# Optimization experiments

Measured on AMD Instinct MI355X. Metric: run time of the kernel, lower is better.

The kernel has to match this reference:

```python
import jax, jax.numpy as jnp
import numpy as np
import math

H = 8  # num_heads
SCALE = 1.0 / math.sqrt(512.0)  # original divides by sqrt(dim_V), not sqrt(head_dim)


def setup_inputs() -> dict:
    key = jax.random.key(0)
    ks = jax.random.split(key, 16)
    B, N, D = 32, 512, 512
    s = 1.0 / math.sqrt(D)
    return {
        "Q": jax.random.normal(ks[0], (B, N, D), jnp.float32),
        "K": jax.random.normal(ks[1], (B, N, D), jnp.float32),
        "Wq": jax.random.normal(ks[2], (D, D), jnp.float32) * s,
        "bq": jnp.zeros((D,), jnp.float32),
        "Wk": jax.random.normal(ks[3], (D, D), jnp.float32) * s,
        "bk": jnp.zeros((D,), jnp.float32),
        "Wv": jax.random.normal(ks[4], (D, D), jnp.float32) * s,
        "bv": jnp.zeros((D,), jnp.float32),
        "Wo": jax.random.normal(ks[5], (D, D), jnp.float32) * s,
        "bo": jnp.zeros((D,), jnp.float32),
        "W1": jax.random.normal(ks[6], (D, D), jnp.float32) * s,
        "b1": jnp.zeros((D,), jnp.float32),
        "W2": jax.random.normal(ks[7], (D, D), jnp.float32) * s,
        "b2": jnp.zeros((D,), jnp.float32),
    }


def reference(Q, K, Wq, bq, Wk, bk, Wv, bv, Wo, bo, W1, b1, W2, b2):
    B, Nq, D = Q.shape
    dh = D // H
    # projections (torch Linear: x @ W.T + b)
    q = (Q @ Wq.T + bq).reshape(B, Nq, H, dh)
    k = (K @ Wk.T + bk).reshape(B, K.shape[1], H, dh)
    v = (K @ Wv.T + bv).reshape(B, K.shape[1], H, dh)
    # scores: [B, H, Nq, Nk], scaled by 1/sqrt(dim_V)
    scores = jnp.einsum("bqhd,bkhd->bhqk", q, k) * SCALE
    # NOTE: original softmax is over dim=1 of [H*B, Nq, Nk] == the QUERY axis
    A = jax.nn.softmax(scores, axis=2)
    attn = jnp.einsum("bhqk,bkhd->bqhd", A, v).reshape(B, Nq, D)
    out = Q + (attn @ Wo.T + bo)  # dropout p=0.0
    ffn = jax.nn.relu(out @ W1.T + b1) @ W2.T + b2
    return out + ffn
```

## Files before the change

kernel.cpp:

```cpp
#include <hip/hip_runtime.h>
#include <stdint.h>

#define SCALE_ 0.044194173824159216f
#define QSC_ (0.044194173824159216f * 1.4426950408889634f)

typedef __attribute__((ext_vector_type(8))) short bf16x8;
typedef __attribute__((ext_vector_type(4))) float f32x4;
typedef __attribute__((ext_vector_type(16))) float f32x16;
typedef __attribute__((ext_vector_type(2))) unsigned int uint2v;

__device__ __forceinline__ ushort f2b(float f) {
  union { float f; uint32_t u; } v; v.f = f;
  return (ushort)((v.u + 0x7fffu + ((v.u >> 16) & 1u)) >> 16);
}
__device__ __forceinline__ uint32_t cvtpk(float lo, float hi) {
  uint32_t r; asm("v_cvt_pk_bf16_f32 %0, %1, %2" : "=v"(r) : "v"(lo), "v"(hi)); return r;
}
__device__ __forceinline__ float ex2(float x) {
  float r; asm("v_exp_f32 %0, %1" : "=v"(r) : "v"(x)); return r;
}
__device__ __forceinline__ void gld16(void* lds, const void* g) {
  __builtin_amdgcn_global_load_lds(
      (const __attribute__((address_space(1))) uint32_t*)g,
      (__attribute__((address_space(3))) uint32_t*)lds, 16, 0, 0);
}

__global__ __launch_bounds__(256)
void k_cvtw(const float* __restrict__ w0, const float* __restrict__ w1,
            const float* __restrict__ w2, const float* __restrict__ w3,
            const float* __restrict__ w4, const float* __restrict__ w5,
            ushort* __restrict__ Wb)
{
  const int NW = 262144;
  int i = (blockIdx.x * 256 + threadIdx.x) * 4;
  int seg = i >> 18;
  int off = i & (NW - 1);
  const float* src;
  switch (seg) { case 0: src = w0; break; case 1: src = w1; break; case 2: src = w2; break;
                 case 3: src = w3; break; case 4: src = w4; break; default: src = w5; }
  float4 v = *(const float4*)(src + off);
  ushort4 o = make_ushort4(f2b(v.x), f2b(v.y), f2b(v.z), f2b(v.w));
  *(ushort4*)(Wb + (size_t)seg * NW + off) = o;
}

template<int EPI>
__device__ __forceinline__ void gemm_body(const ushort* __restrict__ A, const ushort* __restrict__ Bw,
                                          const float* __restrict__ bias, const float* __restrict__ extra,
                                          float* __restrict__ outf, ushort* __restrict__ outb,
                                          char* lds, int m0, int n0)
{
  const int t = threadIdx.x;
  const int w = t >> 6, lane = t & 63;
  const int wm = w >> 1, wn = w & 1;
  const int rA = lane & 15, g = lane >> 4;

  const ushort* srcA[4]; int ldsA[4];
#pragma unroll
  for (int j = 0; j < 4; j++) {
    int L = (t + j*512) * 16;
    int U = L ^ (((L >> 7) & 7) << 4);
    srcA[j] = A + (size_t)(m0 + (U >> 7))*512 + ((U & 127) >> 1);
    ldsA[j] = L;
  }
  const ushort* srcB[2]; int ldsB[2];
#pragma unroll
  for (int j = 0; j < 2; j++) {
    int L = (t + j*512) * 16;
    int U = L ^ (((L >> 7) & 7) << 4);
    srcB[j] = Bw + (size_t)(n0 + (U >> 7))*512 + ((U & 127) >> 1);
    ldsB[j] = 32768 + L;
  }

#define STAGE_T(ti) do { char* bb_ = lds + ((ti) % 3) * 49152; \
    _Pragma("unroll") \
    for (int j = 0; j < 4; j++) gld16(bb_ + ldsA[j], srcA[j] + (ti)*64); \
    _Pragma("unroll") \
    for (int j = 0; j < 2; j++) gld16(bb_ + ldsB[j], srcB[j] + (ti)*64); } while (0)

  STAGE_T(0); STAGE_T(1);

  f32x4 acc[4][4] = {};
  for (int i = 0; i < 8; i++) {
    if (i < 7) asm volatile("s_waitcnt vmcnt(6)" ::: "memory");
    else       asm volatile("s_waitcnt vmcnt(0)" ::: "memory");
    __builtin_amdgcn_s_barrier();
    __builtin_amdgcn_sched_barrier(0);
    const char* bufc = lds + (i % 3) * 49152;

    bf16x8 afA[4], bfA[4], afB[4], bfB[4];
#pragma unroll
    for (int m = 0; m < 4; m++) {
      int row = wm*64 + m*16 + rA;
      afA[m] = *(const bf16x8*)(bufc + ((row*128 + g*16) ^ ((row & 7) << 4)));
      afB[m] = *(const bf16x8*)(bufc + ((row*128 + 64 + g*16) ^ ((row & 7) << 4)));
    }
#pragma unroll
    for (int n = 0; n < 4; n++) {
      int row = wn*64 + n*16 + rA;
      bfA[n] = *(const bf16x8*)(bufc + 32768 + ((row*128 + g*16) ^ ((row & 7) << 4)));
      bfB[n] = *(const bf16x8*)(bufc + 32768 + ((row*128 + 64 + g*16) ^ ((row & 7) << 4)));
    }
    if (i < 6) STAGE_T(i + 2);
    __builtin_amdgcn_sched_barrier(0);
    __builtin_amdgcn_s_setprio(1);
#pragma unroll
    for (int m = 0; m < 4; m++)
#pragma unroll
      for (int n = 0; n < 4; n++)
        acc[m][n] = __builtin_amdgcn_mfma_f32_16x16x32_bf16(afA[m], bfA[n], acc[m][n], 0, 0, 0);
#pragma unroll
    for (int m = 0; m < 4; m++)
#pragma unroll
      for (int n = 0; n < 4; n++)
        acc[m][n] = __builtin_amdgcn_mfma_f32_16x16x32_bf16(afB[m], bfB[n], acc[m][n], 0, 0, 0);
    __builtin_amdgcn_s_setprio(0);
  }
#undef STAGE_T

#pragma unroll
  for (int m = 0; m < 4; m++)
#pragma unroll
    for (int n = 0; n < 4; n++) {
      int col = n0 + wn*64 + n*16 + rA;
      float bb = bias[col];
#pragma unroll
      for (int r = 0; r < 4; r++) {
        int row = m0 + wm*64 + m*16 + g*4 + r;
        size_t idx = (size_t)row*512 + col;
        float v = acc[m][n][r] + bb;
        if (EPI == 1)      { float o = extra[idx] + v; outf[idx] = o; outb[idx] = f2b(o); }
        else if (EPI == 2) outb[idx] = f2b(v > 0.f ? v : 0.f);
        else               outf[idx] += v;
      }
    }
}

template<int EPI>
__global__ __launch_bounds__(512, 2)
void k_gemm(const ushort* __restrict__ A, const ushort* __restrict__ Bw,
            const float* __restrict__ bias, const float* __restrict__ extra,
            float* __restrict__ outf, ushort* __restrict__ outb)
{
  __shared__ __align__(16) char lds[3*49152];
  gemm_body<EPI>(A, Bw, bias, extra, outf, outb, lds, blockIdx.x*256, blockIdx.y*128);
}

template<int DUAL>
__device__ __forceinline__ void proj_body(const float* __restrict__ A32, const ushort* __restrict__ B0w,
                                          const ushort* __restrict__ B1w,
                                          const float* __restrict__ bias0, const float* __restrict__ bias1,
                                          ushort* __restrict__ out0, ushort* __restrict__ vpT,
                                          char* lds, int m0, int n0, float os)
{
  const int t = threadIdx.x;
  const int w = t >> 6, lane = t & 63;
  const int wm = w >> 1, wn = w & 1;
  const int rA = lane & 15, g = lane >> 4;
  const int BUF = DUAL ? 49152 : 40960;
  const int L = DUAL ? 6 : 5;

  const float* srcA[4]; int ldsA[4];
#pragma unroll
  for (int j = 0; j < 4; j++) {
    int Lb = (t + j*512) * 16;
    int U = Lb ^ (((Lb >> 7) & 7) << 4);
    srcA[j] = A32 + (size_t)(m0 + (U >> 7))*512 + ((U & 127) >> 2);
    ldsA[j] = Lb;
  }
  const ushort* srcB0; const ushort* srcB1; int ldsB;
  {
    int Lb = t * 16;
    int U = Lb ^ (((Lb >> 6) & 3) << 4);
    int row = U >> 6, col = (U & 63) >> 1;
    srcB0 = B0w + (size_t)(n0 + row)*512 + col;
    srcB1 = DUAL ? (B1w + (size_t)(n0 + row)*512 + col) : srcB0;
    ldsB = 32768 + Lb;
  }

#define PSTAGE(ti) do { char* bb_ = lds + ((ti) % 3) * BUF; \
    _Pragma("unroll") \
    for (int j = 0; j < 4; j++) gld16(bb_ + ldsA[j], srcA[j] + (ti)*32); \
    gld16(bb_ + ldsB, srcB0 + (ti)*32); \
    if (DUAL) gld16(bb_ + 8192 + ldsB, srcB1 + (ti)*32); } while (0)

  PSTAGE(0); PSTAGE(1);

  f32x4 acc0[4][4] = {};
  f32x4 acc1[4][4] = {};
  for (int i = 0; i < 16; i++) {
    if (i < 15) { if (DUAL) asm volatile("s_waitcnt vmcnt(6)" ::: "memory");
                  else      asm volatile("s_waitcnt vmcnt(5)" ::: "memory"); }
    else          asm volatile("s_waitcnt vmcnt(0)" ::: "memory");
    __builtin_amdgcn_s_barrier();
    __builtin_amdgcn_sched_barrier(0);
    const char* bufc = lds + (i % 3) * BUF;

    bf16x8 af[4];
#pragma unroll
    for (int m = 0; m < 4; m++) {
      int row = wm*64 + m*16 + rA;
      int o0 = (row*128 + g*32) ^ ((row & 7) << 4);
      f32x4 lo = *(const f32x4*)(bufc + o0);
      f32x4 hi = *(const f32x4*)(bufc + (o0 ^ 16));
      union { uint32_t u[4]; bf16x8 v; } af_;
      af_.u[0] = cvtpk(lo[0], lo[1]); af_.u[1] = cvtpk(lo[2], lo[3]);
      af_.u[2] = cvtpk(hi[0], hi[1]); af_.u[3] = cvtpk(hi[2], hi[3]);
      af[m] = af_.v;
    }
    bf16x8 bf0[4];
#pragma unroll
    for (int n = 0; n < 4; n++) {
      int row = wn*64 + n*16 + rA;
      bf0[n] = *(const bf16x8*)(bufc + 32768 + ((row*64 + g*16) ^ ((row & 3) << 4)));
    }
    if (i < 14) PSTAGE(i + 2);
    __builtin_amdgcn_sched_barrier(0);
    __builtin_amdgcn_s_setprio(1);
#pragma unroll
    for (int m = 0; m < 4; m++)
#pragma unroll
      for (int n = 0; n < 4; n++)
        acc0[m][n] = __builtin_amdgcn_mfma_f32_16x16x32_bf16(af[m], bf0[n], acc0[m][n], 0, 0, 0);
    __builtin_amdgcn_s_setprio(0);
    if (DUAL) {
      bf16x8 bf1[4];
#pragma unroll
      for (int n = 0; n < 4; n++) {
        int row = wn*64 + n*16 + rA;
        bf1[n] = *(const bf16x8*)(bufc + 40960 + ((row*64 + g*16) ^ ((row & 3) << 4)));
      }
      __builtin_amdgcn_s_setprio(1);
#pragma unroll
      for (int m = 0; m < 4; m++)
#pragma unroll
        for (int n = 0; n < 4; n++)
          acc1[m][n] = __builtin_amdgcn_mfma_f32_16x16x32_bf16(af[m], bf1[n], acc1[m][n], 0, 0, 0);
      __builtin_amdgcn_s_setprio(0);
    }
  }
#undef PSTAGE

#pragma unroll
  for (int m = 0; m < 4; m++)
#pragma unroll
    for (int n = 0; n < 4; n++) {
      int col = n0 + wn*64 + n*16 + rA;
      {
        float bb = bias0[col];
#pragma unroll
        for (int r = 0; r < 4; r++) {
          int row = m0 + wm*64 + m*16 + g*4 + r;
          out0[(size_t)row*512 + col] = f2b((acc0[m][n][r] + bb) * os);
        }
      }
      if (DUAL) {
        float bb = bias1[col];
        int b = m0 >> 9, k0 = m0 & 511;
        int hh = col >> 6, dl = col & 63;
        int kg = k0 + wm*64 + m*16 + g*4;
        float v0 = acc1[m][n][0] + bb, v1 = acc1[m][n][1] + bb;
        float v2 = acc1[m][n][2] + bb, v3 = acc1[m][n][3] + bb;
        uint2 pk;
        pk.x = (uint32_t)f2b(v0) | ((uint32_t)f2b(v1) << 16);
        pk.y = (uint32_t)f2b(v2) | ((uint32_t)f2b(v3) << 16);
        *(uint2*)(vpT + ((size_t)((b*8 + hh)*64 + dl)*512 + kg)) = pk;
      }
    }
}

__global__ __launch_bounds__(512, 1)
void k_projq(const float* __restrict__ Qf, const ushort* __restrict__ Wb,
             const float* __restrict__ bq, ushort* __restrict__ qp)
{
  __shared__ __align__(16) char lds[3*40960];
  proj_body<0>(Qf, Wb, nullptr, bq, nullptr, qp, nullptr,
               lds, blockIdx.x*256, blockIdx.y*128, QSC_);
}

__global__ __launch_bounds__(512, 1)
void k_projkv(const float* __restrict__ Kf, const ushort* __restrict__ Wb,
              const float* __restrict__ bk, const float* __restrict__ bvv,
              ushort* __restrict__ kp, ushort* __restrict__ vpT)
{
  __shared__ __align__(16) char lds[3*49152];
  proj_body<1>(Kf, Wb + (size_t)262144, Wb + 2*(size_t)262144, bk, bvv, kp, vpT,
               lds, blockIdx.x*256, blockIdx.y*128, 1.0f);
}

__global__ __launch_bounds__(512, 2)
void k_att2(const ushort* __restrict__ qp, const ushort* __restrict__ kp,
            const ushort* __restrict__ vpT, float* __restrict__ zinv,
            ushort* __restrict__ attn)
{
  __shared__ __align__(16) char kt[65536];
  __shared__ __align__(16) char vt[65536];
  __shared__ __align__(16) char qpr[32768];
  int bh = blockIdx.x;
  int b = bh >> 3, h = bh & 7;
  int t = threadIdx.x, w = t >> 6, lane = t & 63;
  int rA = lane & 15, g = lane >> 4;
  const ushort* kbase = kp + (size_t)(b*512)*512 + h*64;
  const ushort* qbase = qp + (size_t)(b*512)*512 + h*64;
  const ushort* vbase = vpT + (size_t)bh*64*512;

#pragma unroll
  for (int i = 0; i < 8; i++) {
    int c = i*512 + t; int row = c >> 3, sl = c & 7;
    gld16(kt + c*16, kbase + (size_t)row*512 + ((sl ^ (row & 7))*8));
  }
#define STAGE_Q(buf, qb) do { \
    _Pragma("unroll") \
    for (int i = 0; i < 2; i++) { \
      int c = i*512 + t; int row = c >> 3, sl = c & 7; \
      gld16(qpr + (buf)*16384 + c*16, \
            qbase + (size_t)((qb)*128 + row)*512 + ((sl ^ (row & 7))*8)); } } while (0)
  STAGE_Q(0, 0);
  STAGE_Q(1, 1);
#pragma unroll
  for (int i = 0; i < 8; i++) {
    int c = i*512 + t; int d = c >> 6, sl = c & 63;
    gld16(vt + c*16, vbase + (size_t)d*512 + ((sl ^ (d & 7))*8));
  }

  asm volatile("s_waitcnt vmcnt(10)" ::: "memory");
  __builtin_amdgcn_s_barrier();
  __builtin_amdgcn_sched_barrier(0);
  bf16x8 kf[4][2];
#pragma unroll
  for (int n = 0; n < 4; n++)
#pragma unroll
    for (int ks = 0; ks < 2; ks++) {
      int k = w*64 + n*16 + rA;
      kf[n][ks] = *(const bf16x8*)(kt + k*128 + (((ks*4 + g) ^ (k & 7))*16));
    }
  float Zacc[4] = {0.f, 0.f, 0.f, 0.f};
  for (int qb = 0; qb < 4; qb++) {
    if (qb == 1)      { asm volatile("s_waitcnt vmcnt(10)" ::: "memory"); }
    else if (qb == 2) { asm volatile("s_waitcnt vmcnt(2)" ::: "memory"); }
    else if (qb == 3) { asm volatile("s_waitcnt vmcnt(0)" ::: "memory"); }
    if (qb) { __builtin_amdgcn_s_barrier(); __builtin_amdgcn_sched_barrier(0); }
    const char* qtb = qpr + (qb & 1)*16384;
    f32x4 acc[8][4] = {};
#pragma unroll
    for (int ks = 0; ks < 2; ks++) {
      bf16x8 af[8];
#pragma unroll
      for (int m = 0; m < 8; m++) {
        int q = m*16 + rA;
        af[m] = *(const bf16x8*)(qtb + q*128 + (((ks*4 + g) ^ (q & 7))*16));
      }
      __builtin_amdgcn_s_setprio(1);
#pragma unroll
      for (int m = 0; m < 8; m++)
#pragma unroll
        for (int n = 0; n < 4; n++)
          acc[m][n] = __builtin_amdgcn_mfma_f32_16x16x32_bf16(af[m], kf[n][ks], acc[m][n], 0, 0, 0);
      __builtin_amdgcn_s_setprio(0);
    }
    if (qb < 3) __builtin_amdgcn_s_barrier();
    if (qb < 2) STAGE_Q(qb & 1, qb + 2);
#pragma unroll
    for (int m = 0; m < 8; m++)
#pragma unroll
      for (int n = 0; n < 4; n++) {
        float s = 0.f;
#pragma unroll
        for (int r = 0; r < 4; r++) s += ex2(acc[m][n][r]);
        Zacc[n] += s;
      }
  }
#undef STAGE_Q
#pragma unroll
  for (int n = 0; n < 4; n++) {
    float v = Zacc[n];
    v += __shfl_xor(v, 16);
    v += __shfl_xor(v, 32);
    if (lane < 16) ((float*)qpr)[w*64 + n*16 + lane] = 1.0f / v;
  }
  __syncthreads();

  const int l31 = lane & 31, hi5 = lane >> 5;
  bf16x8 qf2[2][4];
#pragma unroll
  for (int qb = 0; qb < 2; qb++)
#pragma unroll
    for (int ksd = 0; ksd < 4; ksd++)
      qf2[qb][ksd] = *(const bf16x8*)(qbase + (size_t)(w*64 + qb*32 + l31)*512 + ksd*16 + hi5*8);
  const float* zl = (const float*)qpr;
  f32x16 oacc[2][2] = {};
  for (int kc = 0; kc < 16; kc++) {
    bf16x8 kf2[4];
#pragma unroll
    for (int ksd = 0; ksd < 4; ksd++) {
      int k = kc*32 + l31;
      kf2[ksd] = *(const bf16x8*)(kt + k*128 + (((ksd*2 + hi5) ^ (k & 7))*16));
    }
    bf16x8 vf2[2][2];
#pragma unroll
    for (int db = 0; db < 2; db++)
#pragma unroll
      for (int ks = 0; ks < 2; ks++) {
        int d = db*32 + l31;
        vf2[db][ks] = *(const bf16x8*)(vt + d*1024 + (((kc*4 + ks*2 + hi5) ^ (d & 7))*16));
      }
    f32x4 zv[4];
#pragma unroll
    for (int j = 0; j < 4; j++)
      zv[j] = *(const f32x4*)(zl + kc*32 + j*8 + hi5*4);
#pragma unroll
    for (int qb = 0; qb < 2; qb++) {
      f32x16 s = {};
      __builtin_amdgcn_s_setprio(1);
#pragma unroll
      for (int ksd = 0; ksd < 4; ksd++)
        s = __builtin_amdgcn_mfma_f32_32x32x16_bf16(kf2[ksd], qf2[qb][ksd], s, 0, 0, 0);
      __builtin_amdgcn_s_setprio(0);
      float e[16];
#pragma unroll
      for (int r = 0; r < 16; r++) e[r] = ex2(s[r]) * zv[r >> 2][r & 3];
      uint32_t x0 = cvtpk(e[0], e[1]),   y0 = cvtpk(e[4], e[5]);
      uint32_t x1 = cvtpk(e[2], e[3]),   y1 = cvtpk(e[6], e[7]);
      uint32_t x2 = cvtpk(e[8], e[9]),   y2 = cvtpk(e[12], e[13]);
      uint32_t x3 = cvtpk(e[10], e[11]), y3 = cvtpk(e[14], e[15]);
      uint2v r0 = __builtin_amdgcn_permlane32_swap(x0, y0, false, false);
      uint2v r1 = __builtin_amdgcn_permlane32_swap(x1, y1, false, false);
      uint2v r2 = __builtin_amdgcn_permlane32_swap(x2, y2, false, false);
      uint2v r3 = __builtin_amdgcn_permlane32_swap(x3, y3, false, false);
      union { uint32_t u[4]; bf16x8 v; } p0, p1;
      p0.u[0] = r0[0]; p0.u[1] = r1[0]; p0.u[2] = r0[1]; p0.u[3] = r1[1];
      p1.u[0] = r2[0]; p1.u[1] = r3[0]; p1.u[2] = r2[1]; p1.u[3] = r3[1];
      __builtin_amdgcn_s_setprio(1);
#pragma unroll
      for (int db = 0; db < 2; db++) {
        oacc[qb][db] = __builtin_amdgcn_mfma_f32_32x32x16_bf16(p0.v, vf2[db][0], oacc[qb][db], 0, 0, 0);
        oacc[qb][db] = __builtin_amdgcn_mfma_f32_32x32x16_bf16(p1.v, vf2[db][1], oacc[qb][db], 0, 0, 0);
      }
      __builtin_amdgcn_s_setprio(0);
    }
  }
#pragma unroll
  for (int qb = 0; qb < 2; qb++)
#pragma unroll
    for (int db = 0; db < 2; db++)
#pragma unroll
      for (int r = 0; r < 16; r++) {
        int q = w*64 + qb*32 + (r & 3) + 8*(r >> 2) + 4*hi5;
        int d = db*32 + l31;
        attn[(size_t)(b*512 + q)*512 + h*64 + d] = f2b(oacc[qb][db][r]);
      }
}

extern "C" void kernel_launch(void* const* d_in, const int* in_sizes, int n_in,
                              void* d_out, int out_size, void* d_ws, size_t ws_size,
                              hipStream_t stream) {
  const float* Q  = (const float*)d_in[0];
  const float* K  = (const float*)d_in[1];
  const float* Wq = (const float*)d_in[2];
  const float* bq = (const float*)d_in[3];
  const float* Wk = (const float*)d_in[4];
  const float* bk = (const float*)d_in[5];
  const float* Wv = (const float*)d_in[6];
  const float* bv = (const float*)d_in[7];
  const float* Wo = (const float*)d_in[8];
  const float* bo = (const float*)d_in[9];
  const float* W1 = (const float*)d_in[10];
  const float* b1 = (const float*)d_in[11];
  const float* W2 = (const float*)d_in[12];
  const float* b2 = (const float*)d_in[13];
  float* out = (float*)d_out;

  const size_t SZ = (size_t)16384 * 512;
  ushort* attn = (ushort*)d_ws;
  ushort* outb = attn + SZ;
  ushort* qp   = outb + SZ;
  ushort* kp   = qp + SZ;
  ushort* vpT  = kp + SZ;
  ushort* Wb   = vpT + SZ;
  float*  zinv = (float*)(Wb + 6 * (size_t)262144);
  ushort* h1   = vpT;

  k_cvtw<<<dim3(1536), dim3(256), 0, stream>>>(Wq, Wk, Wv, Wo, W1, W2, Wb);
  k_projq<<<dim3(64, 4), dim3(512), 0, stream>>>(Q, Wb, bq, qp);
  k_projkv<<<dim3(64, 4), dim3(512), 0, stream>>>(K, Wb, bk, bv, kp, vpT);
  k_att2<<<dim3(256), dim3(512), 0, stream>>>(qp, kp, vpT, zinv, attn);
  k_gemm<1><<<dim3(64, 4), dim3(512), 0, stream>>>(attn, Wb + 3*(size_t)262144, bo, Q, out, outb);
  k_gemm<2><<<dim3(64, 4), dim3(512), 0, stream>>>(outb, Wb + 4*(size_t)262144, b1, nullptr, nullptr, h1);
  k_gemm<3><<<dim3(64, 4), dim3(512), 0, stream>>>(h1, Wb + 5*(size_t)262144, b2, nullptr, out, nullptr);
}
```

Measured before the change: 141.7 us.

## Merge Q/KV projection launches, read Q/V from global in attention, retune B swizzle

Fuses the Q and KV projection kernels into one launch with a z dimension, so both projections can run concurrently across the GPU. The attention kernel drops its LDS staging of Q and V. It now loads those fragments straight from global memory, with only K and the normalizer kept in LDS, which cuts shared memory use and may allow more resident blocks. The B-tile LDS swizzle in the projection is changed to use a different row bit pattern to reduce bank conflicts. The risk is that the global loads in the attention inner loops are uncoalesced and uncached, adding latency.

```diff
diff --git a/kernel.cpp b/kernel.cpp
--- a/kernel.cpp
+++ b/kernel.cpp
@@ -157,7 +157,6 @@
   const int wm = w >> 1, wn = w & 1;
   const int rA = lane & 15, g = lane >> 4;
   const int BUF = DUAL ? 49152 : 40960;
-  const int L = DUAL ? 6 : 5;
 
   const float* srcA[4]; int ldsA[4];
 #pragma unroll
@@ -170,7 +169,7 @@
   const ushort* srcB0; const ushort* srcB1; int ldsB;
   {
     int Lb = t * 16;
-    int U = Lb ^ (((Lb >> 6) & 3) << 4);
+    int U = Lb ^ (((Lb >> 7) & 3) << 4);
     int row = U >> 6, col = (U & 63) >> 1;
     srcB0 = B0w + (size_t)(n0 + row)*512 + col;
     srcB1 = DUAL ? (B1w + (size_t)(n0 + row)*512 + col) : srcB0;
@@ -211,7 +210,7 @@
 #pragma unroll
     for (int n = 0; n < 4; n++) {
       int row = wn*64 + n*16 + rA;
-      bf0[n] = *(const bf16x8*)(bufc + 32768 + ((row*64 + g*16) ^ ((row & 3) << 4)));
+      bf0[n] = *(const bf16x8*)(bufc + 32768 + ((row*64 + g*16) ^ (((row >> 1) & 3) << 4)));
     }
     if (i < 14) PSTAGE(i + 2);
     __builtin_amdgcn_sched_barrier(0);
@@ -227,7 +226,7 @@
 #pragma unroll
       for (int n = 0; n < 4; n++) {
         int row = wn*64 + n*16 + rA;
-        bf1[n] = *(const bf16x8*)(bufc + 40960 + ((row*64 + g*16) ^ ((row & 3) << 4)));
+        bf1[n] = *(const bf16x8*)(bufc + 40960 + ((row*64 + g*16) ^ (((row >> 1) & 3) << 4)));
       }
       __builtin_amdgcn_s_setprio(1);
 #pragma unroll
@@ -269,32 +268,28 @@
 }
 
 __global__ __launch_bounds__(512, 1)
-void k_projq(const float* __restrict__ Qf, const ushort* __restrict__ Wb,
-             const float* __restrict__ bq, ushort* __restrict__ qp)
-{
-  __shared__ __align__(16) char lds[3*40960];
-  proj_body<0>(Qf, Wb, nullptr, bq, nullptr, qp, nullptr,
-               lds, blockIdx.x*256, blockIdx.y*128, QSC_);
-}
-
-__global__ __launch_bounds__(512, 1)
-void k_projkv(const float* __restrict__ Kf, const ushort* __restrict__ Wb,
-              const float* __restrict__ bk, const float* __restrict__ bvv,
-              ushort* __restrict__ kp, ushort* __restrict__ vpT)
+void k_proj(const float* __restrict__ Qf, const float* __restrict__ Kf,
+            const ushort* __restrict__ Wb,
+            const float* __restrict__ bq, const float* __restrict__ bk,
+            const float* __restrict__ bvv,
+            ushort* __restrict__ qp, ushort* __restrict__ kp, ushort* __restrict__ vpT)
 {
   __shared__ __align__(16) char lds[3*49152];
-  proj_body<1>(Kf, Wb + (size_t)262144, Wb + 2*(size_t)262144, bk, bvv, kp, vpT,
-               lds, blockIdx.x*256, blockIdx.y*128, 1.0f);
+  if (blockIdx.z == 0) {
+    proj_body<0>(Qf, Wb, nullptr, bq, nullptr, qp, nullptr,
+                 lds, blockIdx.x*256, blockIdx.y*128, QSC_);
+  } else {
+    proj_body<1>(Kf, Wb + (size_t)262144, Wb + 2*(size_t)262144, bk, bvv, kp, vpT,
+                 lds, blockIdx.x*256, blockIdx.y*128, 1.0f);
+  }
 }
 
 __global__ __launch_bounds__(512, 2)
 void k_att2(const ushort* __restrict__ qp, const ushort* __restrict__ kp,
-            const ushort* __restrict__ vpT, float* __restrict__ zinv,
-            ushort* __restrict__ attn)
+            const ushort* __restrict__ vpT, ushort* __restrict__ attn)
 {
   __shared__ __align__(16) char kt[65536];
-  __shared__ __align__(16) char vt[65536];
-  __shared__ __align__(16) char qpr[32768];
+  __shared__ __align__(16) float zl[512];
   int bh = blockIdx.x;
   int b = bh >> 3, h = bh & 7;
   int t = threadIdx.x, w = t >> 6, lane = t & 63;
@@ -308,23 +303,10 @@
     int c = i*512 + t; int row = c >> 3, sl = c & 7;
     gld16(kt + c*16, kbase + (size_t)row*512 + ((sl ^ (row & 7))*8));
   }
-#define STAGE_Q(buf, qb) do { \
-    _Pragma("unroll") \
-    for (int i = 0; i < 2; i++) { \
-      int c = i*512 + t; int row = c >> 3, sl = c & 7; \
-      gld16(qpr + (buf)*16384 + c*16, \
-            qbase + (size_t)((qb)*128 + row)*512 + ((sl ^ (row & 7))*8)); } } while (0)
-  STAGE_Q(0, 0);
-  STAGE_Q(1, 1);
-#pragma unroll
-  for (int i = 0; i < 8; i++) {
-    int c = i*512 + t; int d = c >> 6, sl = c & 63;
-    gld16(vt + c*16, vbase + (size_t)d*512 + ((sl ^ (d & 7))*8));
-  }
-
-  asm volatile("s_waitcnt vmcnt(10)" ::: "memory");
+  asm volatile("s_waitcnt vmcnt(0)" ::: "memory");
   __builtin_amdgcn_s_barrier();
   __builtin_amdgcn_sched_barrier(0);
+
   bf16x8 kf[4][2];
 #pragma unroll
   for (int n = 0; n < 4; n++)
@@ -334,20 +316,16 @@
       kf[n][ks] = *(const bf16x8*)(kt + k*128 + (((ks*4 + g) ^ (k & 7))*16));
     }
   float Zacc[4] = {0.f, 0.f, 0.f, 0.f};
+#pragma unroll 1
   for (int qb = 0; qb < 4; qb++) {
-    if (qb == 1)      { asm volatile("s_waitcnt vmcnt(10)" ::: "memory"); }
-    else if (qb == 2) { asm volatile("s_waitcnt vmcnt(2)" ::: "memory"); }
-    else if (qb == 3) { asm volatile("s_waitcnt vmcnt(0)" ::: "memory"); }
-    if (qb) { __builtin_amdgcn_s_barrier(); __builtin_amdgcn_sched_barrier(0); }
-    const char* qtb = qpr + (qb & 1)*16384;
     f32x4 acc[8][4] = {};
 #pragma unroll
     for (int ks = 0; ks < 2; ks++) {
       bf16x8 af[8];
 #pragma unroll
       for (int m = 0; m < 8; m++) {
-        int q = m*16 + rA;
-        af[m] = *(const bf16x8*)(qtb + q*128 + (((ks*4 + g) ^ (q & 7))*16));
+        int q = qb*128 + m*16 + rA;
+        af[m] = *(const bf16x8*)(qbase + (size_t)q*512 + ks*32 + g*8);
       }
       __builtin_amdgcn_s_setprio(1);
 #pragma unroll
@@ -357,8 +335,6 @@
           acc[m][n] = __builtin_amdgcn_mfma_f32_16x16x32_bf16(af[m], kf[n][ks], acc[m][n], 0, 0, 0);
       __builtin_amdgcn_s_setprio(0);
     }
-    if (qb < 3) __builtin_amdgcn_s_barrier();
-    if (qb < 2) STAGE_Q(qb & 1, qb + 2);
 #pragma unroll
     for (int m = 0; m < 8; m++)
 #pragma unroll
@@ -369,13 +345,12 @@
         Zacc[n] += s;
       }
   }
-#undef STAGE_Q
 #pragma unroll
   for (int n = 0; n < 4; n++) {
     float v = Zacc[n];
     v += __shfl_xor(v, 16);
     v += __shfl_xor(v, 32);
-    if (lane < 16) ((float*)qpr)[w*64 + n*16 + lane] = 1.0f / v;
+    if (lane < 16) zl[w*64 + n*16 + lane] = 1.0f / v;
   }
   __syncthreads();
 
@@ -386,8 +361,8 @@
 #pragma unroll
     for (int ksd = 0; ksd < 4; ksd++)
       qf2[qb][ksd] = *(const bf16x8*)(qbase + (size_t)(w*64 + qb*32 + l31)*512 + ksd*16 + hi5*8);
-  const float* zl = (const float*)qpr;
   f32x16 oacc[2][2] = {};
+#pragma unroll 1
   for (int kc = 0; kc < 16; kc++) {
     bf16x8 kf2[4];
 #pragma unroll
@@ -401,12 +376,12 @@
 #pragma unroll
       for (int ks = 0; ks < 2; ks++) {
         int d = db*32 + l31;
-        vf2[db][ks] = *(const bf16x8*)(vt + d*1024 + (((kc*4 + ks*2 + hi5) ^ (d & 7))*16));
+        vf2[db][ks] = *(const bf16x8*)(vbase + (size_t)d*512 + kc*32 + ks*16 + hi5*8);
       }
     f32x4 zv[4];
 #pragma unroll
     for (int j = 0; j < 4; j++)
-      zv[j] = *(const f32x4*)(zl + kc*32 + j*8 + hi5*4);
+      zv[j] = *(const f32x4*)(&zl[kc*32 + j*8 + hi5*4]);
 #pragma unroll
     for (int qb = 0; qb < 2; qb++) {
       f32x16 s = {};
@@ -476,13 +451,11 @@
   ushort* kp   = qp + SZ;
   ushort* vpT  = kp + SZ;
   ushort* Wb   = vpT + SZ;
-  float*  zinv = (float*)(Wb + 6 * (size_t)262144);
   ushort* h1   = vpT;
 
   k_cvtw<<<dim3(1536), dim3(256), 0, stream>>>(Wq, Wk, Wv, Wo, W1, W2, Wb);
-  k_projq<<<dim3(64, 4), dim3(512), 0, stream>>>(Q, Wb, bq, qp);
-  k_projkv<<<dim3(64, 4), dim3(512), 0, stream>>>(K, Wb, bk, bv, kp, vpT);
-  k_att2<<<dim3(256), dim3(512), 0, stream>>>(qp, kp, vpT, zinv, attn);
+  k_proj<<<dim3(64, 4, 2), dim3(512), 0, stream>>>(Q, K, Wb, bq, bk, bv, qp, kp, vpT);
+  k_att2<<<dim3(256), dim3(512), 0, stream>>>(qp, kp, vpT, attn);
   k_gemm<1><<<dim3(64, 4), dim3(512), 0, stream>>>(attn, Wb + 3*(size_t)262144, bo, Q, out, outb);
   k_gemm<2><<<dim3(64, 4), dim3(512), 0, stream>>>(outb, Wb + 4*(size_t)262144, b1, nullptr, nullptr, h1);
   k_gemm<3><<<dim3(64, 4), dim3(512), 0, stream>>>(h1, Wb + 5*(size_t)262144, b2, nullptr, out, nullptr);
```

After: 144.2 us. About the same (+1.8%).
